# Kernel optimization log

Hardware: AMD Instinct MI355X
Metric: run time of the kernel (lower is better)

Reference implementation:

```python
import jax, jax.numpy as jnp
import numpy as np

NEG = -1000000000.0  # mask value used by the original module

def setup_inputs() -> dict:
    key = jax.random.key(0)
    kq, kk, kv, kl = jax.random.split(key, 4)
    B, Lq, Lk, D, Dv = 16, 2048, 2048, 64, 64
    q = jax.random.normal(kq, (B, Lq, D), dtype=jnp.float32)
    k = jax.random.normal(kk, (B, Lk, D), dtype=jnp.float32)
    v = jax.random.normal(kv, (B, Lk, Dv), dtype=jnp.float32)
    valid_len = jax.random.randint(kl, (B, Lq), 0, Lk, dtype=jnp.int32)
    return {"q": q, "k": k, "v": v, "valid_len": valid_len}

def reference(q, k, v, valid_len):
    # scores: [B, Lq, Lk]  (NOTE: original module does NOT scale by sqrt(d))
    scores = jnp.einsum('bqd,bkd->bqk', q, k)
    Lk = k.shape[1]
    # per-(batch,query) valid length masking over the key dimension
    mask = jnp.arange(Lk, dtype=valid_len.dtype)[None, None, :] < valid_len[:, :, None]
    scores = jnp.where(mask, scores, NEG)
    attn = jax.nn.softmax(scores, axis=-1)
    # dropout p=0.0 -> identity
    return jnp.einsum('bqk,bkv->bqv', attn, v)
```

## Files before the change

### kernel.cpp

```cpp
#include <hip/hip_runtime.h>

typedef _Float16 f16;
typedef __attribute__((ext_vector_type(8))) _Float16 f16x8;
typedef __attribute__((ext_vector_type(4))) _Float16 f16x4;
typedef __attribute__((ext_vector_type(4))) float f32x4;

#define NB 16
#define LSEQ 2048
#define DIM 64
#define KVB 64
#define QT 64
#define NT (LSEQ / KVB)
#define PITCH 72
#define LOG2E 1.44269504088896340736f

__device__ inline f16x4 pkcvt(const f32x4 x) {
    auto a = __builtin_amdgcn_cvt_pkrtz(x[0], x[1]);
    auto b = __builtin_amdgcn_cvt_pkrtz(x[2], x[3]);
    f16x4 t; t[0]=(f16)a[0]; t[1]=(f16)a[1]; t[2]=(f16)b[0]; t[3]=(f16)b[1];
    return t;
}

__device__ inline void gload16(const void* g, void* l) {
    __builtin_amdgcn_global_load_lds(
        (const __attribute__((address_space(1))) unsigned int*)g,
        (__attribute__((address_space(3))) unsigned int*)l, 16, 0, 0);
}

__global__ void build_perm(const int* __restrict__ vlg, int* __restrict__ perm) {
    const int b = blockIdx.x, tid = threadIdx.x;
    __shared__ int hist[NT + 1];
    __shared__ int base[NT + 1];
    if (tid <= NT) hist[tid] = 0;
    __syncthreads();
    for (int q = tid; q < LSEQ; q += 256) {
        int vl = vlg[b * LSEQ + q];
        int t = (vl == 0) ? NT : ((vl + KVB - 1) >> 6);
        atomicAdd(&hist[t], 1);
    }
    __syncthreads();
    if (tid == 0) {
        int acc = 0;
        for (int t = NT; t >= 0; --t) { base[t] = acc; acc += hist[t]; }
    }
    __syncthreads();
    for (int q = tid; q < LSEQ; q += 256) {
        int vl = vlg[b * LSEQ + q];
        int t = (vl == 0) ? NT : ((vl + KVB - 1) >> 6);
        int pos = atomicAdd(&base[t], 1);
        perm[b * LSEQ + pos] = q;
    }
}

__global__ __launch_bounds__(256) void kvprep(
    const float* __restrict__ kg, const float* __restrict__ vg,
    f16* __restrict__ k16, f16* __restrict__ v16)
{
    const int bt = blockIdx.x;
    const int b = bt >> 5, t = bt & 31;
    const int tid = threadIdx.x;
    const float* kb_ = kg + ((size_t)b * LSEQ + t * KVB) * DIM;
    const float* vb_ = vg + ((size_t)b * LSEQ + t * KVB) * DIM;
    f16* kd = k16 + (size_t)bt * (KVB * DIM);
    f16* vd = v16 + (size_t)bt * (KVB * DIM);
#pragma unroll
    for (int it = 0; it < 4; ++it) {
        int cc = tid + it * 256;
        int row = cc >> 4, c4 = (cc & 15) * 4;
        f32x4 x = *(const f32x4*)(kb_ + row * DIM + c4);
        *(f16x4*)(kd + row * 64 + (c4 ^ ((row & 7) * 8))) = pkcvt(x);
    }
    {
        int kb4 = tid & 15, dvb = tid >> 4;
        f32x4 rr[4];
#pragma unroll
        for (int i = 0; i < 4; ++i)
            rr[i] = *(const f32x4*)(vb_ + (size_t)(kb4 * 4 + i) * DIM + dvb * 4);
#pragma unroll
        for (int j = 0; j < 4; ++j) {
            int dv = dvb * 4 + j;
            f32x4 col = {rr[0][j], rr[1][j], rr[2][j], rr[3][j]};
            *(f16x4*)(vd + dv * 64 + ((kb4 * 4) ^ ((dv & 7) * 8))) = pkcvt(col);
        }
    }
}

__global__ __launch_bounds__(256, 3) void attn_fwd(
    const float* __restrict__ qg, const int* __restrict__ vlg,
    const f16* __restrict__ k16, const f16* __restrict__ v16,
    float* __restrict__ outg, const int* __restrict__ perm,
    f16* __restrict__ opart, float* __restrict__ mlg, int S)
{
    __shared__ alignas(16) f16 kbuf[2][KVB * 64];
    __shared__ alignas(16) f16 vbuf[2][DIM * 64];
    __shared__ alignas(16) f16 pld[4 * 16 * PITCH];
    __shared__ int wmax[4];

    const int tid  = threadIdx.x;
    const int wid  = tid >> 6;
    const int lane = tid & 63;
    const int r    = lane & 15;
    const int hi   = lane >> 4;

    const int bid = blockIdx.x;
    const int nbs = NB * S;
    const int qt  = bid / nbs;
    const int rem = bid - qt * nbs;
    const int b   = rem / S;
    const int s   = rem - b * S;
    const int qw  = qt * QT + wid * 16;

    const int qidx = perm[b * LSEQ + qw + r];
    const int vl   = vlg[b * LSEQ + qidx];

    int tq = (vl == 0) ? NT : ((vl + KVB - 1) >> 6);
    tq = max(tq, __shfl_xor(tq, 1));
    tq = max(tq, __shfl_xor(tq, 2));
    tq = max(tq, __shfl_xor(tq, 4));
    tq = max(tq, __shfl_xor(tq, 8));
    if (lane == 0) wmax[wid] = tq;
    __syncthreads();
    const int maxt = max(max(wmax[0], wmax[1]), max(wmax[2], wmax[3]));

    int vmin = vl;
    vmin = min(vmin, __shfl_xor(vmin, 1));
    vmin = min(vmin, __shfl_xor(vmin, 2));
    vmin = min(vmin, __shfl_xor(vmin, 4));
    vmin = min(vmin, __shfl_xor(vmin, 8));

    f16x8 qf[2];
    const float* qrow = qg + ((size_t)(b * LSEQ + qidx)) * DIM;
#pragma unroll
    for (int ks = 0; ks < 2; ++ks) {
        f32x4 x = *(const f32x4*)(qrow + ks * 32 + hi * 8);
        f32x4 y = *(const f32x4*)(qrow + ks * 32 + hi * 8 + 4);
        f32x4 xs = {x[0]*LOG2E, x[1]*LOG2E, x[2]*LOG2E, x[3]*LOG2E};
        f32x4 ys = {y[0]*LOG2E, y[1]*LOG2E, y[2]*LOG2E, y[3]*LOG2E};
        f16x4 lo = pkcvt(xs), hh = pkcvt(ys);
        f16x8 t;
        t[0]=lo[0]; t[1]=lo[1]; t[2]=lo[2]; t[3]=lo[3];
        t[4]=hh[0]; t[5]=hh[1]; t[6]=hh[2]; t[7]=hh[3];
        qf[ks] = t;
    }

    float m_run = -INFINITY;
    float l_run = 0.0f;
    f32x4 o[4];
#pragma unroll
    for (int dt = 0; dt < 4; ++dt) o[dt] = f32x4{0.f, 0.f, 0.f, 0.f};

    f16* pw = pld + wid * (16 * PITCH);
    const f16* kt_base = k16 + (size_t)b * (NT * KVB * DIM);
    const f16* vt_base = v16 + (size_t)b * (NT * KVB * DIM);
    const int swz = (r & 7) * 8;

    auto stage = [&](int bi, int t) {
        const char* ks = (const char*)(kt_base + (size_t)t * 4096);
        const char* vs = (const char*)(vt_base + (size_t)t * 4096);
        char* kd = (char*)&kbuf[bi][0];
        char* vd = (char*)&vbuf[bi][0];
        gload16(ks + tid * 16,        kd + tid * 16);
        gload16(ks + 4096 + tid * 16, kd + 4096 + tid * 16);
        gload16(vs + tid * 16,        vd + tid * 16);
        gload16(vs + 4096 + tid * 16, vd + 4096 + tid * 16);
    };

    if (s < maxt) stage(0, s);
    int c = 0;
    for (int tt = s; tt < maxt; tt += S) {
        __syncthreads();
        if (tt + S < maxt) stage(c ^ 1, tt + S);

        f32x4 st[4];
        __builtin_amdgcn_s_setprio(1);
#pragma unroll
        for (int kt = 0; kt < 4; ++kt) {
            f32x4 acc = f32x4{0.f, 0.f, 0.f, 0.f};
#pragma unroll
            for (int ks = 0; ks < 2; ++ks) {
                f16x8 kf = *(const f16x8*)(&kbuf[c][(kt * 16 + r) * 64 + ((ks * 32 + hi * 8) ^ swz)]);
                acc = __builtin_amdgcn_mfma_f32_16x16x32_f16(kf, qf[ks], acc, 0, 0, 0);
            }
            st[kt] = acc;
        }
        __builtin_amdgcn_s_setprio(0);

        const int kv0 = tt * KVB;
        float lanemax = -INFINITY;
        if (kv0 + KVB > vmin) {
#pragma unroll
            for (int kt = 0; kt < 4; ++kt)
#pragma unroll
                for (int g = 0; g < 4; ++g) {
                    int key = kv0 + kt * 16 + hi * 4 + g;
                    float sv = (key < vl) ? st[kt][g] : -1e9f;
                    st[kt][g] = sv;
                    lanemax = fmaxf(lanemax, sv);
                }
        } else {
#pragma unroll
            for (int kt = 0; kt < 4; ++kt)
#pragma unroll
                for (int g = 0; g < 4; ++g)
                    lanemax = fmaxf(lanemax, st[kt][g]);
        }

        if (__any(lanemax > m_run + 8.0f)) {
            float tmax = lanemax;
            tmax = fmaxf(tmax, __shfl_xor(tmax, 16));
            tmax = fmaxf(tmax, __shfl_xor(tmax, 32));
            float m_new = fmaxf(m_run, tmax);
            float scale = exp2f(m_run - m_new);
            l_run *= scale;
            m_run = m_new;
#pragma unroll
            for (int g = 0; g < 4; ++g) {
                float sc = __shfl(scale, hi * 4 + g);
#pragma unroll
                for (int dt = 0; dt < 4; ++dt) o[dt][g] *= sc;
            }
        }

#pragma unroll
        for (int kt = 0; kt < 4; ++kt) {
            f16x4 pv;
#pragma unroll
            for (int g = 0; g < 4; ++g) {
                float p = exp2f(st[kt][g] - m_run);
                l_run += p;
                pv[g] = (f16)p;
            }
            *(f16x4*)(pw + r * PITCH + kt * 16 + hi * 4) = pv;
        }

        __builtin_amdgcn_s_setprio(1);
#pragma unroll
        for (int ks = 0; ks < 2; ++ks) {
            f16x8 pa = *(const f16x8*)(pw + r * PITCH + ks * 32 + hi * 8);
#pragma unroll
            for (int dt = 0; dt < 4; ++dt) {
                f16x8 vf = *(const f16x8*)(&vbuf[c][(dt * 16 + r) * 64 + ((ks * 32 + hi * 8) ^ swz)]);
                o[dt] = __builtin_amdgcn_mfma_f32_16x16x32_f16(pa, vf, o[dt], 0, 0, 0);
            }
        }
        __builtin_amdgcn_s_setprio(0);
        c ^= 1;
    }

    l_run += __shfl_xor(l_run, 16);
    l_run += __shfl_xor(l_run, 32);

    if (S == 1) {
        float inv = 1.0f / l_run;
#pragma unroll
        for (int g = 0; g < 4; ++g) {
            float iv = __shfl(inv, hi * 4 + g);
            int   qo = __shfl(qidx, hi * 4 + g);
            float* ob = outg + ((size_t)(b * LSEQ + qo)) * DIM;
#pragma unroll
            for (int dt = 0; dt < 4; ++dt)
                ob[dt * 16 + r] = o[dt][g] * iv;
        }
    } else {
        f16* obase = opart + ((size_t)s * NB * LSEQ + (size_t)b * LSEQ) * DIM;
#pragma unroll
        for (int g = 0; g < 4; ++g) {
            int qo = __shfl(qidx, hi * 4 + g);
            f16* ob = obase + (size_t)qo * DIM;
#pragma unroll
            for (int dt = 0; dt < 4; ++dt)
                ob[dt * 16 + r] = (f16)o[dt][g];
        }
        if (hi == 0) {
            size_t mi = ((size_t)s * NB * LSEQ + (size_t)b * LSEQ + qidx) * 2;
            mlg[mi]     = m_run;
            mlg[mi + 1] = l_run;
        }
    }
}

__global__ void merge_k(const f16* __restrict__ opart, const float* __restrict__ mlg,
                        float* __restrict__ outg, int S)
{
    const int gt = blockIdx.x * 256 + threadIdx.x;
    const size_t base = (size_t)gt * 4;
    const size_t qg = base >> 6;
    float M = -INFINITY;
    for (int s = 0; s < S; ++s)
        M = fmaxf(M, mlg[((size_t)s * NB * LSEQ + qg) * 2]);
    float den = 0.f;
    f32x4 acc = {0.f, 0.f, 0.f, 0.f};
    for (int s = 0; s < S; ++s) {
        size_t mi = ((size_t)s * NB * LSEQ + qg) * 2;
        float w = exp2f(mlg[mi] - M);
        den += w * mlg[mi + 1];
        f16x4 ov = *(const f16x4*)(opart + (size_t)s * (NB * LSEQ * DIM) + base);
        acc[0] += w * (float)ov[0]; acc[1] += w * (float)ov[1];
        acc[2] += w * (float)ov[2]; acc[3] += w * (float)ov[3];
    }
    float inv = 1.0f / den;
    f32x4 res = {acc[0]*inv, acc[1]*inv, acc[2]*inv, acc[3]*inv};
    *(f32x4*)(outg + base) = res;
}

extern "C" void kernel_launch(void* const* d_in, const int* in_sizes, int n_in,
                              void* d_out, int out_size, void* d_ws, size_t ws_size,
                              hipStream_t stream) {
    const float* q  = (const float*)d_in[0];
    const float* k  = (const float*)d_in[1];
    const float* v  = (const float*)d_in[2];
    const int*   vl = (const int*)d_in[3];
    float* out = (float*)d_out;

    const size_t perm_b = (size_t)NB * LSEQ * sizeof(int);
    const size_t kv_b   = (size_t)NB * LSEQ * DIM * sizeof(f16);
    auto need = [&](int S) {
        return perm_b + 2 * kv_b
             + (size_t)S * NB * LSEQ * 2 * sizeof(float)
             + (size_t)S * NB * LSEQ * DIM * sizeof(f16);
    };
    int S;
    if      (ws_size >= need(4)) S = 4;
    else if (ws_size >= need(2)) S = 2;
    else                         S = 1;

    int*   perm  = (int*)d_ws;
    f16*   k16   = (f16*)((char*)d_ws + perm_b);
    f16*   v16   = (f16*)((char*)d_ws + perm_b + kv_b);
    float* mlg   = (float*)((char*)d_ws + perm_b + 2 * kv_b);
    f16*   opart = (f16*)((char*)d_ws + perm_b + 2 * kv_b
                          + (size_t)S * NB * LSEQ * 2 * sizeof(float));

    build_perm<<<NB, 256, 0, stream>>>(vl, perm);
    kvprep<<<NB * NT, 256, 0, stream>>>(k, v, k16, v16);

    attn_fwd<<<dim3(NB * (LSEQ / QT) * S), dim3(256), 0, stream>>>(
        q, vl, k16, v16, out, perm, opart, mlg, S);

    if (S > 1) {
        const int mthreads = NB * LSEQ * DIM / 4;
        merge_k<<<dim3(mthreads / 256), dim3(256), 0, stream>>>(opart, mlg, out, S);
    }
}
```

Baseline: 51.93 us.

## Process two query fragments per wave and fuse perm build into KV prep

Each wave now handles two 16-row query fragments (query tile 128 instead of 64), so every K/V tile staged into LDS is reused by twice as many queries and global K/V traffic per query halves. The histogram-based permutation kernel is folded into the K/V conversion kernel as extra blocks, removing one launch. The cost is higher register pressure from doubled Q fragments and accumulators under launch_bounds(256,3), half as many attention blocks, and a coarser tile bound, because each block now loops to the maximum valid length across 128 sorted queries.

```diff
diff --git a/kernel.cpp b/kernel.cpp
--- a/kernel.cpp
+++ b/kernel.cpp
@@ -9,7 +9,8 @@
 #define LSEQ 2048
 #define DIM 64
 #define KVB 64
-#define QT 64
+#define QT 128
+#define NQT (LSEQ / QT)
 #define NT (LSEQ / KVB)
 #define PITCH 72
 #define LOG2E 1.44269504088896340736f
@@ -27,50 +28,26 @@
         (__attribute__((address_space(3))) unsigned int*)l, 16, 0, 0);
 }
 
-__global__ void build_perm(const int* __restrict__ vlg, int* __restrict__ perm) {
-    const int b = blockIdx.x, tid = threadIdx.x;
-    __shared__ int hist[NT + 1];
-    __shared__ int base[NT + 1];
-    if (tid <= NT) hist[tid] = 0;
-    __syncthreads();
-    for (int q = tid; q < LSEQ; q += 256) {
-        int vl = vlg[b * LSEQ + q];
-        int t = (vl == 0) ? NT : ((vl + KVB - 1) >> 6);
-        atomicAdd(&hist[t], 1);
-    }
-    __syncthreads();
-    if (tid == 0) {
-        int acc = 0;
-        for (int t = NT; t >= 0; --t) { base[t] = acc; acc += hist[t]; }
-    }
-    __syncthreads();
-    for (int q = tid; q < LSEQ; q += 256) {
-        int vl = vlg[b * LSEQ + q];
-        int t = (vl == 0) ? NT : ((vl + KVB - 1) >> 6);
-        int pos = atomicAdd(&base[t], 1);
-        perm[b * LSEQ + pos] = q;
-    }
-}
-
-__global__ __launch_bounds__(256) void kvprep(
+__global__ __launch_bounds__(256) void prep(
     const float* __restrict__ kg, const float* __restrict__ vg,
-    f16* __restrict__ k16, f16* __restrict__ v16)
+    const int* __restrict__ vlg,
+    f16* __restrict__ k16, f16* __restrict__ v16, int* __restrict__ perm)
 {
-    const int bt = blockIdx.x;
-    const int b = bt >> 5, t = bt & 31;
     const int tid = threadIdx.x;
-    const float* kb_ = kg + ((size_t)b * LSEQ + t * KVB) * DIM;
-    const float* vb_ = vg + ((size_t)b * LSEQ + t * KVB) * DIM;
-    f16* kd = k16 + (size_t)bt * (KVB * DIM);
-    f16* vd = v16 + (size_t)bt * (KVB * DIM);
-#pragma unroll
-    for (int it = 0; it < 4; ++it) {
-        int cc = tid + it * 256;
-        int row = cc >> 4, c4 = (cc & 15) * 4;
-        f32x4 x = *(const f32x4*)(kb_ + row * DIM + c4);
-        *(f16x4*)(kd + row * 64 + (c4 ^ ((row & 7) * 8))) = pkcvt(x);
-    }
-    {
+    if (blockIdx.x < NB * NT) {
+        const int bt = blockIdx.x;
+        const int b = bt >> 5, t = bt & 31;
+        const float* kb_ = kg + ((size_t)b * LSEQ + t * KVB) * DIM;
+        const float* vb_ = vg + ((size_t)b * LSEQ + t * KVB) * DIM;
+        f16* kd = k16 + (size_t)bt * (KVB * DIM);
+        f16* vd = v16 + (size_t)bt * (KVB * DIM);
+#pragma unroll
+        for (int it = 0; it < 4; ++it) {
+            int cc = tid + it * 256;
+            int row = cc >> 4, c4 = (cc & 15) * 4;
+            f32x4 x = *(const f32x4*)(kb_ + row * DIM + c4);
+            *(f16x4*)(kd + row * 64 + (c4 ^ ((row & 7) * 8))) = pkcvt(x);
+        }
         int kb4 = tid & 15, dvb = tid >> 4;
         f32x4 rr[4];
 #pragma unroll
@@ -81,6 +58,29 @@
             int dv = dvb * 4 + j;
             f32x4 col = {rr[0][j], rr[1][j], rr[2][j], rr[3][j]};
             *(f16x4*)(vd + dv * 64 + ((kb4 * 4) ^ ((dv & 7) * 8))) = pkcvt(col);
+        }
+    } else {
+        const int b = blockIdx.x - NB * NT;
+        __shared__ int hist[NT + 1];
+        __shared__ int base[NT + 1];
+        if (tid <= NT) hist[tid] = 0;
+        __syncthreads();
+        for (int q = tid; q < LSEQ; q += 256) {
+            int vl = vlg[b * LSEQ + q];
+            int t = (vl == 0) ? NT : ((vl + KVB - 1) >> 6);
+            atomicAdd(&hist[t], 1);
+        }
+        __syncthreads();
+        if (tid == 0) {
+            int acc = 0;
+            for (int t = NT; t >= 0; --t) { base[t] = acc; acc += hist[t]; }
+        }
+        __syncthreads();
+        for (int q = tid; q < LSEQ; q += 256) {
+            int vl = vlg[b * LSEQ + q];
+            int t = (vl == 0) ? NT : ((vl + KVB - 1) >> 6);
+            int pos = atomicAdd(&base[t], 1);
+            perm[b * LSEQ + pos] = q;
         }
     }
 }
@@ -110,10 +110,13 @@
     const int s   = rem - b * S;
     const int qw  = qt * QT + wid * 16;
 
-    const int qidx = perm[b * LSEQ + qw + r];
-    const int vl   = vlg[b * LSEQ + qidx];
-
-    int tq = (vl == 0) ? NT : ((vl + KVB - 1) >> 6);
+    const int qidxA = perm[b * LSEQ + qw + r];
+    const int qidxB = perm[b * LSEQ + qw + 64 + r];
+    const int vlA   = vlg[b * LSEQ + qidxA];
+    const int vlB   = vlg[b * LSEQ + qidxB];
+
+    int tq = max((vlA == 0) ? NT : ((vlA + KVB - 1) >> 6),
+                 (vlB == 0) ? NT : ((vlB + KVB - 1) >> 6));
     tq = max(tq, __shfl_xor(tq, 1));
     tq = max(tq, __shfl_xor(tq, 2));
     tq = max(tq, __shfl_xor(tq, 4));
@@ -122,32 +125,40 @@
     __syncthreads();
     const int maxt = max(max(wmax[0], wmax[1]), max(wmax[2], wmax[3]));
 
-    int vmin = vl;
-    vmin = min(vmin, __shfl_xor(vmin, 1));
-    vmin = min(vmin, __shfl_xor(vmin, 2));
-    vmin = min(vmin, __shfl_xor(vmin, 4));
-    vmin = min(vmin, __shfl_xor(vmin, 8));
-
-    f16x8 qf[2];
-    const float* qrow = qg + ((size_t)(b * LSEQ + qidx)) * DIM;
-#pragma unroll
-    for (int ks = 0; ks < 2; ++ks) {
-        f32x4 x = *(const f32x4*)(qrow + ks * 32 + hi * 8);
-        f32x4 y = *(const f32x4*)(qrow + ks * 32 + hi * 8 + 4);
-        f32x4 xs = {x[0]*LOG2E, x[1]*LOG2E, x[2]*LOG2E, x[3]*LOG2E};
-        f32x4 ys = {y[0]*LOG2E, y[1]*LOG2E, y[2]*LOG2E, y[3]*LOG2E};
-        f16x4 lo = pkcvt(xs), hh = pkcvt(ys);
-        f16x8 t;
-        t[0]=lo[0]; t[1]=lo[1]; t[2]=lo[2]; t[3]=lo[3];
-        t[4]=hh[0]; t[5]=hh[1]; t[6]=hh[2]; t[7]=hh[3];
-        qf[ks] = t;
-    }
-
-    float m_run = -INFINITY;
-    float l_run = 0.0f;
-    f32x4 o[4];
-#pragma unroll
-    for (int dt = 0; dt < 4; ++dt) o[dt] = f32x4{0.f, 0.f, 0.f, 0.f};
+    auto wave_min = [&](int v) {
+        v = min(v, __shfl_xor(v, 1));
+        v = min(v, __shfl_xor(v, 2));
+        v = min(v, __shfl_xor(v, 4));
+        v = min(v, __shfl_xor(v, 8));
+        return v;
+    };
+    const int vminA = wave_min(vlA);
+    const int vminB = wave_min(vlB);
+
+    auto load_q = [&](int qidx, f16x8* qf) {
+        const float* qrow = qg + ((size_t)(b * LSEQ + qidx)) * DIM;
+#pragma unroll
+        for (int ks = 0; ks < 2; ++ks) {
+            f32x4 x = *(const f32x4*)(qrow + ks * 32 + hi * 8);
+            f32x4 y = *(const f32x4*)(qrow + ks * 32 + hi * 8 + 4);
+            f32x4 xs = {x[0]*LOG2E, x[1]*LOG2E, x[2]*LOG2E, x[3]*LOG2E};
+            f32x4 ys = {y[0]*LOG2E, y[1]*LOG2E, y[2]*LOG2E, y[3]*LOG2E};
+            f16x4 lo = pkcvt(xs), hh = pkcvt(ys);
+            f16x8 t;
+            t[0]=lo[0]; t[1]=lo[1]; t[2]=lo[2]; t[3]=lo[3];
+            t[4]=hh[0]; t[5]=hh[1]; t[6]=hh[2]; t[7]=hh[3];
+            qf[ks] = t;
+        }
+    };
+    f16x8 qfA[2], qfB[2];
+    load_q(qidxA, qfA);
+    load_q(qidxB, qfB);
+
+    float mA = -INFINITY, mB = -INFINITY;
+    float lA = 0.0f, lB = 0.0f;
+    f32x4 oA[4], oB[4];
+#pragma unroll
+    for (int dt = 0; dt < 4; ++dt) { oA[dt] = f32x4{0,0,0,0}; oB[dt] = f32x4{0,0,0,0}; }
 
     f16* pw = pld + wid * (16 * PITCH);
     const f16* kt_base = k16 + (size_t)b * (NT * KVB * DIM);
@@ -165,27 +176,23 @@
         gload16(vs + 4096 + tid * 16, vd + 4096 + tid * 16);
     };
 
-    if (s < maxt) stage(0, s);
-    int c = 0;
-    for (int tt = s; tt < maxt; tt += S) {
-        __syncthreads();
-        if (tt + S < maxt) stage(c ^ 1, tt + S);
-
+    auto do_frag = [&](const f16x8* qf, int vl, int vmin,
+                       float& m_run, float& l_run, f32x4* o,
+                       int kv0, const f16* kb_, const f16* vb_) {
         f32x4 st[4];
         __builtin_amdgcn_s_setprio(1);
 #pragma unroll
         for (int kt = 0; kt < 4; ++kt) {
-            f32x4 acc = f32x4{0.f, 0.f, 0.f, 0.f};
+            f32x4 acc = f32x4{0,0,0,0};
 #pragma unroll
             for (int ks = 0; ks < 2; ++ks) {
-                f16x8 kf = *(const f16x8*)(&kbuf[c][(kt * 16 + r) * 64 + ((ks * 32 + hi * 8) ^ swz)]);
+                f16x8 kf = *(const f16x8*)(&kb_[(kt * 16 + r) * 64 + ((ks * 32 + hi * 8) ^ swz)]);
                 acc = __builtin_amdgcn_mfma_f32_16x16x32_f16(kf, qf[ks], acc, 0, 0, 0);
             }
             st[kt] = acc;
         }
         __builtin_amdgcn_s_setprio(0);
 
-        const int kv0 = tt * KVB;
         float lanemax = -INFINITY;
         if (kv0 + KVB > vmin) {
 #pragma unroll
@@ -239,44 +246,57 @@
             f16x8 pa = *(const f16x8*)(pw + r * PITCH + ks * 32 + hi * 8);
 #pragma unroll
             for (int dt = 0; dt < 4; ++dt) {
-                f16x8 vf = *(const f16x8*)(&vbuf[c][(dt * 16 + r) * 64 + ((ks * 32 + hi * 8) ^ swz)]);
+                f16x8 vf = *(const f16x8*)(&vb_[(dt * 16 + r) * 64 + ((ks * 32 + hi * 8) ^ swz)]);
                 o[dt] = __builtin_amdgcn_mfma_f32_16x16x32_f16(pa, vf, o[dt], 0, 0, 0);
             }
         }
         __builtin_amdgcn_s_setprio(0);
+    };
+
+    if (s < maxt) stage(0, s);
+    int c = 0;
+    for (int tt = s; tt < maxt; tt += S) {
+        __syncthreads();
+        if (tt + S < maxt) stage(c ^ 1, tt + S);
+        const int kv0 = tt * KVB;
+        do_frag(qfA, vlA, vminA, mA, lA, oA, kv0, &kbuf[c][0], &vbuf[c][0]);
+        do_frag(qfB, vlB, vminB, mB, lB, oB, kv0, &kbuf[c][0], &vbuf[c][0]);
         c ^= 1;
     }
 
-    l_run += __shfl_xor(l_run, 16);
-    l_run += __shfl_xor(l_run, 32);
-
-    if (S == 1) {
-        float inv = 1.0f / l_run;
-#pragma unroll
-        for (int g = 0; g < 4; ++g) {
-            float iv = __shfl(inv, hi * 4 + g);
-            int   qo = __shfl(qidx, hi * 4 + g);
-            float* ob = outg + ((size_t)(b * LSEQ + qo)) * DIM;
-#pragma unroll
-            for (int dt = 0; dt < 4; ++dt)
-                ob[dt * 16 + r] = o[dt][g] * iv;
-        }
-    } else {
-        f16* obase = opart + ((size_t)s * NB * LSEQ + (size_t)b * LSEQ) * DIM;
-#pragma unroll
-        for (int g = 0; g < 4; ++g) {
-            int qo = __shfl(qidx, hi * 4 + g);
-            f16* ob = obase + (size_t)qo * DIM;
-#pragma unroll
-            for (int dt = 0; dt < 4; ++dt)
-                ob[dt * 16 + r] = (f16)o[dt][g];
-        }
-        if (hi == 0) {
-            size_t mi = ((size_t)s * NB * LSEQ + (size_t)b * LSEQ + qidx) * 2;
-            mlg[mi]     = m_run;
-            mlg[mi + 1] = l_run;
-        }
-    }
+    auto epi = [&](float m_run, float l_run, f32x4* o, int qidx) {
+        l_run += __shfl_xor(l_run, 16);
+        l_run += __shfl_xor(l_run, 32);
+        if (S == 1) {
+            float inv = 1.0f / l_run;
+#pragma unroll
+            for (int g = 0; g < 4; ++g) {
+                float iv = __shfl(inv, hi * 4 + g);
+                int   qo = __shfl(qidx, hi * 4 + g);
+                float* ob = outg + ((size_t)(b * LSEQ + qo)) * DIM;
+#pragma unroll
+                for (int dt = 0; dt < 4; ++dt)
+                    ob[dt * 16 + r] = o[dt][g] * iv;
+            }
+        } else {
+            f16* obase = opart + ((size_t)s * NB * LSEQ + (size_t)b * LSEQ) * DIM;
+#pragma unroll
+            for (int g = 0; g < 4; ++g) {
+                int qo = __shfl(qidx, hi * 4 + g);
+                f16* ob = obase + (size_t)qo * DIM;
+#pragma unroll
+                for (int dt = 0; dt < 4; ++dt)
+                    ob[dt * 16 + r] = (f16)o[dt][g];
+            }
+            if (hi == 0) {
+                size_t mi = ((size_t)s * NB * LSEQ + (size_t)b * LSEQ + qidx) * 2;
+                mlg[mi]     = m_run;
+                mlg[mi + 1] = l_run;
+            }
+        }
+    };
+    epi(mA, lA, oA, qidxA);
+    epi(mB, lB, oB, qidxB);
 }
 
 __global__ void merge_k(const f16* __restrict__ opart, const float* __restrict__ mlg,
@@ -331,10 +351,9 @@
     f16*   opart = (f16*)((char*)d_ws + perm_b + 2 * kv_b
                           + (size_t)S * NB * LSEQ * 2 * sizeof(float));
 
-    build_perm<<<NB, 256, 0, stream>>>(vl, perm);
-    kvprep<<<NB * NT, 256, 0, stream>>>(k, v, k16, v16);
-
-    attn_fwd<<<dim3(NB * (LSEQ / QT) * S), dim3(256), 0, stream>>>(
+    prep<<<NB * NT + NB, 256, 0, stream>>>(k, v, vl, k16, v16, perm);
+
+    attn_fwd<<<dim3(NQT * NB * S), dim3(256), 0, stream>>>(
         q, vl, k16, v16, out, perm, opart, mlg, S);
 
     if (S > 1) {
```

After: 51.16 us. Within noise of the previous version (-1.5%).
